# Optimization experiments

Measured on AMD Instinct MI355X. Metric: run time of the kernel, lower is better.

The kernel has to match this reference:

```python
import jax, jax.numpy as jnp
import numpy as np

QN = 127.0  # 2^(8-1)-1, symmetric int8
EPS = 1e-5  # batchnorm eps

def ste_round(v):
    return v + jax.lax.stop_gradient(jnp.round(v) - v)

def quant_act(x):
    # HAWQ-style symmetric per-tensor activation quantization (8-bit)
    s = jnp.maximum(jnp.max(jnp.abs(x)) / QN, 1e-8)
    xq = jnp.clip(ste_round(x / s), -QN - 1.0, QN)
    return xq * s, s

def setup_inputs() -> dict:
    key = jax.random.key(0)
    k1, k2, k3, k4, k5, k6 = jax.random.split(key, 6)
    B, Cin, Cout, H, W = 128, 768, 192, 17, 17
    x = jax.random.normal(k1, (B, Cin, H, W), dtype=jnp.float32)
    conv_w = jax.random.normal(k2, (Cout, Cin, 1, 1), dtype=jnp.float32) * 0.02
    bn_gamma = 1.0 + 0.1 * jax.random.normal(k3, (Cout,), dtype=jnp.float32)
    bn_beta = 0.1 * jax.random.normal(k4, (Cout,), dtype=jnp.float32)
    bn_mean = 0.1 * jax.random.normal(k5, (Cout,), dtype=jnp.float32)
    bn_var = 0.5 + jax.random.uniform(k6, (Cout,), dtype=jnp.float32)
    return {"x": x, "conv_w": conv_w, "bn_gamma": bn_gamma, "bn_beta": bn_beta,
            "bn_mean": bn_mean, "bn_var": bn_var, "cluster": 0}

def reference(x, conv_w, bn_gamma, bn_beta, bn_mean, bn_var, cluster):
    # 1) QuantAct on raw input
    x1, s0 = quant_act(x)
    # 2) QuantAveragePool2d (k=3, s=1, p=1, count_include_pad=True): pool in integer domain
    x_int = ste_round(x1 / s0)
    pooled_sum = jax.lax.reduce_window(x_int, 0.0, jax.lax.add,
                                       (1, 1, 3, 3), (1, 1, 1, 1),
                                       [(0, 0), (0, 0), (1, 1), (1, 1)])
    x2 = (pooled_sum / 9.0) * s0
    # 3) QuantAct after pool
    x3, s1 = quant_act(x2)
    # 4) QuantBnConv2d: fold BN into 1x1 conv, per-channel symmetric weight quant
    std = jnp.sqrt(bn_var + EPS)
    w_fold = conv_w * (bn_gamma / std)[:, None, None, None]          # [O,C,1,1]
    b_fold = bn_beta - bn_gamma * bn_mean / std                      # [O]
    w_sf = jnp.maximum(jnp.max(jnp.abs(w_fold), axis=(1, 2, 3)) / QN, 1e-8)  # [O]
    w_int = jnp.clip(ste_round(w_fold / w_sf[:, None, None, None]), -QN - 1.0, QN)
    xi = x3 / s1                                                     # integer-valued acts
    b_int = ste_round(b_fold / (w_sf * s1))
    out_int = jnp.einsum('bchw,oc->bohw', xi, w_int[:, :, 0, 0]) + b_int[None, :, None, None]
    out = out_int * (w_sf * s1)[None, :, None, None]
    # 5) ReLU + output QuantAct
    out = jax.nn.relu(out)
    outq, s2 = quant_act(out)
    return outq, s2
```

## Files before the change

### kernel.cpp

```cpp
#include <hip/hip_runtime.h>
#include <math.h>

#define B_    128
#define C_    768
#define O_    192
#define HW_   289
#define N_IN  (128*768*289)
#define N_OUT (128*192*289)
#define QN_   127.0f

#define SLAB_E   (32*289)
#define SLAB_SH  9248
#define SLAB_BYT 18496
#define QP_LDS   (32*380)

typedef __attribute__((ext_vector_type(8))) short bf16x8;
typedef __attribute__((ext_vector_type(4))) float f32x4;

#define SWZ(b) ((b) ^ ((((b) >> 6) & 3) << 4))


__global__ void k_absmax_x(const float4* __restrict__ x4, int n4, unsigned* cnt) {
    float m = 0.f;
    const int stride = gridDim.x * blockDim.x;
    int i = blockIdx.x * blockDim.x + threadIdx.x;
    for (; i + stride < n4; i += 2 * stride) {
        float4 v = x4[i];
        float4 w = x4[i + stride];
        m = fmaxf(m, fmaxf(fmaxf(fabsf(v.x), fabsf(v.y)),
                           fmaxf(fabsf(v.z), fabsf(v.w))));
        m = fmaxf(m, fmaxf(fmaxf(fabsf(w.x), fabsf(w.y)),
                           fmaxf(fabsf(w.z), fabsf(w.w))));
    }
    if (i < n4) {
        float4 v = x4[i];
        m = fmaxf(m, fmaxf(fmaxf(fabsf(v.x), fabsf(v.y)),
                           fmaxf(fabsf(v.z), fabsf(v.w))));
    }
#pragma unroll
    for (int off = 32; off; off >>= 1) m = fmaxf(m, __shfl_down(m, off));
    __shared__ float sm[4];
    int lane = threadIdx.x & 63, wv = threadIdx.x >> 6;
    if (lane == 0) sm[wv] = m;
    __syncthreads();
    if (threadIdx.x == 0) {
        float bm = fmaxf(fmaxf(sm[0], sm[1]), fmaxf(sm[2], sm[3]));
        atomicMax(cnt + 0, __float_as_uint(bm));
    }
}

__launch_bounds__(512) __global__
void k_quant_pool(const float* __restrict__ x, short* __restrict__ pooled,
                  unsigned* cnt) {
    __shared__ __align__(16) float fq[QP_LDS + 8];
    __shared__ int smax[8];
    const int tid = threadIdx.x;
    const int kt = blockIdx.x;
    const int b = blockIdx.z;
    const float s0 = fmaxf(__uint_as_float(cnt[0]) / QN_, 1e-8f);

    for (int i = tid; i < QP_LDS + 8; i += 512) fq[i] = 0.f;
    __syncthreads();

    const float4* xg4 = (const float4*)(x + ((size_t)b * 768 + kt * 32) * HW_);
    for (int t = tid; t < SLAB_E / 4; t += 512) {
        float4 v = xg4[t];
        float q0 = rintf(v.x / s0);
        float q1 = rintf(v.y / s0);
        float q2 = rintf(v.z / s0);
        float q3 = rintf(v.w / s0);
        int e = 4 * t;
#pragma unroll
        for (int j = 0; j < 4; ++j) {
            float q = (j == 0) ? q0 : (j == 1) ? q1 : (j == 2) ? q2 : q3;
            int ej = e + j;
            int p = (ej * 29027) >> 23;
            int i2 = ej - p * 289;
            int r = (i2 * 3856) >> 16;
            int c = i2 - r * 17;
            fq[p * 380 + (r + 1) * 20 + (c + 1)] = q;
        }
    }
    __syncthreads();

    short* slab = pooled + (size_t)(b * 24 + kt) * SLAB_SH;
    int tmax = 0;
    for (int task = tid; task < 2720; task += 512) {
        int p = task & 31;
        int rt = task >> 5;
        int r = (rt * 3277) >> 14;
        int t5 = rt - r * 5;
        int c0 = t5 * 4;
        const float* base = fq + p * 380 + r * 20 + c0;
        float4 a0 = *(const float4*)(base);
        float4 a1 = *(const float4*)(base + 4);
        float4 b0 = *(const float4*)(base + 20);
        float4 b1 = *(const float4*)(base + 24);
        float4 d0 = *(const float4*)(base + 40);
        float4 d1 = *(const float4*)(base + 44);
        float s0c = a0.x + b0.x + d0.x;
        float s1c = a0.y + b0.y + d0.y;
        float s2c = a0.z + b0.z + d0.z;
        float s3c = a0.w + b0.w + d0.w;
        float s4c = a1.x + b1.x + d1.x;
        float s5c = a1.y + b1.y + d1.y;
        int o0 = (int)(s0c + s1c + s2c);
        int o1 = (int)(s1c + s2c + s3c);
        int o2 = (int)(s2c + s3c + s4c);
        int o3 = (int)(s3c + s4c + s5c);
        int i0 = r * 17 + c0;
        slab[(i0 + 0) * 32 + p] = (short)o0;
        int a = o0 < 0 ? -o0 : o0; tmax = a > tmax ? a : tmax;
        if (c0 + 1 < 17) {
            slab[(i0 + 1) * 32 + p] = (short)o1;
            a = o1 < 0 ? -o1 : o1; tmax = a > tmax ? a : tmax;
            slab[(i0 + 2) * 32 + p] = (short)o2;
            a = o2 < 0 ? -o2 : o2; tmax = a > tmax ? a : tmax;
            slab[(i0 + 3) * 32 + p] = (short)o3;
            a = o3 < 0 ? -o3 : o3; tmax = a > tmax ? a : tmax;
        }
    }

#pragma unroll
    for (int off = 32; off; off >>= 1) {
        int o = __shfl_down(tmax, off);
        tmax = o > tmax ? o : tmax;
    }
    if ((tid & 63) == 0) smax[tid >> 6] = tmax;
    __syncthreads();
    if (tid == 0) {
        int bm = smax[0];
#pragma unroll
        for (int i = 1; i < 8; ++i) bm = smax[i] > bm ? smax[i] : bm;
        atomicMax((int*)(cnt + 1), bm);
    }
}

__global__ void k_weights(const float* __restrict__ conv_w,
                          const float* __restrict__ g,
                          const float* __restrict__ beta,
                          const float* __restrict__ mu,
                          const float* __restrict__ var,
                          const unsigned* __restrict__ cnt,
                          unsigned short* __restrict__ w_q,
                          float* __restrict__ b_int, float* __restrict__ scale_o,
                          unsigned short* __restrict__ lut) {
    if (blockIdx.x == O_) {
        const float s0 = fmaxf(__uint_as_float(cnt[0]) / QN_, 1e-8f);
        const float maxx2 = ((float)((const int*)cnt)[1] / 9.0f) * s0;
        const float s1 = fmaxf(maxx2 / QN_, 1e-8f);
        for (int i = threadIdx.x; i < 2305; i += 256) {
            float p = (float)(i - 1152);
            float t = (p / 9.0f) * s0;
            float v = rintf(t / s1);
            v = fminf(fmaxf(v, -128.f), 127.f);
            lut[i] = (unsigned short)(__float_as_uint(v) >> 16);
        }
        return;
    }
    const int o = blockIdx.x;
    const float stdv = sqrtf(var[o] + 1e-5f);
    const float r = g[o] / stdv;
    const float* wo = conv_w + o * C_;
    float m = 0.f;
    for (int c = threadIdx.x; c < C_; c += 256) m = fmaxf(m, fabsf(wo[c] * r));
#pragma unroll
    for (int off = 32; off; off >>= 1) m = fmaxf(m, __shfl_down(m, off));
    __shared__ float sm[4];
    __shared__ float swsf;
    int lane = threadIdx.x & 63, wv = threadIdx.x >> 6;
    if (lane == 0) sm[wv] = m;
    __syncthreads();
    if (threadIdx.x == 0) {
        float bm = fmaxf(fmaxf(sm[0], sm[1]), fmaxf(sm[2], sm[3]));
        swsf = fmaxf(bm / QN_, 1e-8f);
    }
    __syncthreads();
    const float wsf = swsf;
    for (int c = threadIdx.x; c < C_; c += 256) {
        float wi = rintf(wo[c] * r / wsf);
        wi = fminf(fmaxf(wi, -128.f), 127.f);
        w_q[(c >> 5) * 6144 + o * 32 + (c & 31)] =
            (unsigned short)(__float_as_uint(wi) >> 16);
    }
    if (threadIdx.x == 0) {
        float s0 = fmaxf(__uint_as_float(cnt[0]) / QN_, 1e-8f);
        float maxx2 = ((float)((const int*)cnt)[1] / 9.0f) * s0;
        float s1 = fmaxf(maxx2 / QN_, 1e-8f);
        float bf = beta[o] - g[o] * mu[o] / stdv;
        b_int[o] = rintf(bf / (wsf * s1));
        scale_o[o] = wsf * s1;
    }
}

__global__ void k_xi(uint4* __restrict__ data,
                     const unsigned short* __restrict__ lut_g) {
    __shared__ unsigned short s_lut[2305];
    for (int i = threadIdx.x; i < 2305; i += 256) s_lut[i] = lut_g[i];
    __syncthreads();
    const int n4 = N_IN / 8;
    for (int i = blockIdx.x * blockDim.x + threadIdx.x; i < n4;
         i += gridDim.x * blockDim.x) {
        uint4 v = data[i];
        uint4 o;
        o.x = (unsigned)s_lut[1152 + (short)(v.x)] |
              ((unsigned)s_lut[1152 + (short)(v.x >> 16)] << 16);
        o.y = (unsigned)s_lut[1152 + (short)(v.y)] |
              ((unsigned)s_lut[1152 + (short)(v.y >> 16)] << 16);
        o.z = (unsigned)s_lut[1152 + (short)(v.z)] |
              ((unsigned)s_lut[1152 + (short)(v.z >> 16)] << 16);
        o.w = (unsigned)s_lut[1152 + (short)(v.w)] |
              ((unsigned)s_lut[1152 + (short)(v.w >> 16)] << 16);
        data[i] = o;
    }
}

__launch_bounds__(256) __global__
void k_gemm(const unsigned short* __restrict__ xi,
            const unsigned short* __restrict__ w_q,
            const float* __restrict__ b_int, const float* __restrict__ scale_o,
            unsigned* cnt, float* __restrict__ out) {
    __shared__ char sW[2][12288];
    __shared__ char sX[2][5120];
    __shared__ float red[4];
    const int tid = threadIdx.x;
    const int b = blockIdx.z;
    const int hw0 = blockIdx.x * 80;
    const int L = tid & 63;
    const int wv = tid >> 6;
    const int wo = wv * 48;
    const char* xi_b = (const char*)xi;

    const int dA = wv * 1024 + L * 16;
    const int rowA = min(hw0 + (dA >> 6), HW_ - 1);
    const int offA = rowA * 64 + ((dA & 63) ^ (((dA >> 6) & 3) << 4));
    const int dB = 4096 + L * 16;
    const int rowB = min(hw0 + (dB >> 6), HW_ - 1);
    const int offB = rowB * 64 + ((dB & 63) ^ (((dB >> 6) & 3) << 4));

    auto stageW = [&](int kt, int buf) {
#pragma unroll
        for (int j = 0; j < 3; ++j) {
            int ldsoff = (wv * 3 + j) * 1024;
            const char* src = (const char*)w_q + kt * 12288 + SWZ(ldsoff + L * 16);
            __builtin_amdgcn_global_load_lds(
                (const __attribute__((address_space(1))) unsigned int*)src,
                (__attribute__((address_space(3))) unsigned int*)(&sW[buf][0] + ldsoff),
                16, 0, 0);
        }
    };
    auto stageX = [&](int kt, int buf) {
        size_t slab = (size_t)(b * 24 + kt) * SLAB_BYT;
        __builtin_amdgcn_global_load_lds(
            (const __attribute__((address_space(1))) unsigned int*)(xi_b + slab + offA),
            (__attribute__((address_space(3))) unsigned int*)(&sX[buf][0] + wv * 1024),
            16, 0, 0);
        if (wv == 0) {
            __builtin_amdgcn_global_load_lds(
                (const __attribute__((address_space(1))) unsigned int*)(xi_b + slab + offB),
                (__attribute__((address_space(3))) unsigned int*)(&sX[buf][0] + 4096),
                16, 0, 0);
        }
    };

    f32x4 acc[3][5] = {};

    stageW(0, 0);
    stageX(0, 0);
    __syncthreads();

    for (int kt = 0; kt < 24; ++kt) {
        const int cur = kt & 1, nxt = cur ^ 1;
        if (kt < 23) {
            stageW(kt + 1, nxt);
            stageX(kt + 1, nxt);
        }
        bf16x8 af[3], bfr[5];
#pragma unroll
        for (int m = 0; m < 3; ++m)
            af[m] = *(const bf16x8*)(&sW[cur][0] +
                SWZ((wo + m * 16 + (L & 15)) * 64 + (L >> 4) * 16));
#pragma unroll
        for (int n = 0; n < 5; ++n)
            bfr[n] = *(const bf16x8*)(&sX[cur][0] +
                SWZ((n * 16 + (L & 15)) * 64 + (L >> 4) * 16));
#pragma unroll
        for (int m = 0; m < 3; ++m)
#pragma unroll
            for (int n = 0; n < 5; ++n)
                acc[m][n] = __builtin_amdgcn_mfma_f32_16x16x32_bf16(
                    af[m], bfr[n], acc[m][n], 0, 0, 0);
        __syncthreads();
    }

    float lmax = 0.f;
#pragma unroll
    for (int m = 0; m < 3; ++m) {
        int ob = wo + m * 16 + (L >> 4) * 4;
        float bi0 = b_int[ob + 0], bi1 = b_int[ob + 1];
        float bi2 = b_int[ob + 2], bi3 = b_int[ob + 3];
        float sc0 = scale_o[ob + 0], sc1 = scale_o[ob + 1];
        float sc2 = scale_o[ob + 2], sc3 = scale_o[ob + 3];
#pragma unroll
        for (int n = 0; n < 5; ++n) {
            int hw = hw0 + n * 16 + (L & 15);
            if (hw < HW_) {
                size_t base = ((size_t)b * O_ + ob) * HW_ + hw;
                float v0 = fmaxf((acc[m][n][0] + bi0) * sc0, 0.f);
                float v1 = fmaxf((acc[m][n][1] + bi1) * sc1, 0.f);
                float v2 = fmaxf((acc[m][n][2] + bi2) * sc2, 0.f);
                float v3 = fmaxf((acc[m][n][3] + bi3) * sc3, 0.f);
                out[base + 0 * HW_] = v0;
                out[base + 1 * HW_] = v1;
                out[base + 2 * HW_] = v2;
                out[base + 3 * HW_] = v3;
                lmax = fmaxf(fmaxf(fmaxf(v0, v1), fmaxf(v2, v3)), lmax);
            }
        }
    }
#pragma unroll
    for (int off = 32; off; off >>= 1) lmax = fmaxf(lmax, __shfl_down(lmax, off));
    if (L == 0) red[wv] = lmax;
    __syncthreads();
    if (tid == 0) {
        float bm = fmaxf(fmaxf(red[0], red[1]), fmaxf(red[2], red[3]));
        atomicMax(cnt + 2, __float_as_uint(bm));
    }
}

__global__ void k_quant_out(float* __restrict__ out, const unsigned* __restrict__ cnt) {
    const float s2 = fmaxf(__uint_as_float(cnt[2]) / QN_, 1e-8f);
    float4* o4 = (float4*)out;
    const int n4 = N_OUT / 4;
    for (int i = blockIdx.x * blockDim.x + threadIdx.x; i < n4;
         i += gridDim.x * blockDim.x) {
        float4 v = o4[i];
        v.x = fminf(fmaxf(rintf(v.x / s2), -128.f), 127.f) * s2;
        v.y = fminf(fmaxf(rintf(v.y / s2), -128.f), 127.f) * s2;
        v.z = fminf(fmaxf(rintf(v.z / s2), -128.f), 127.f) * s2;
        v.w = fminf(fmaxf(rintf(v.w / s2), -128.f), 127.f) * s2;
        o4[i] = v;
    }
    if (blockIdx.x == 0 && threadIdx.x == 0) out[N_OUT] = s2;
}

extern "C" void kernel_launch(void* const* d_in, const int* in_sizes, int n_in,
                              void* d_out, int out_size, void* d_ws, size_t ws_size,
                              hipStream_t stream) {
    const float* x      = (const float*)d_in[0];
    const float* conv_w = (const float*)d_in[1];
    const float* g      = (const float*)d_in[2];
    const float* beta   = (const float*)d_in[3];
    const float* mu     = (const float*)d_in[4];
    const float* var    = (const float*)d_in[5];
    float* out = (float*)d_out;

    char* wsb = (char*)d_ws;
    unsigned* cnt          = (unsigned*)wsb;
    float* b_int           = (float*)(wsb + 1024);
    float* scale_o         = (float*)(wsb + 2048);
    unsigned short* lut    = (unsigned short*)(wsb + 3072);
    unsigned short* w_q    = (unsigned short*)(wsb + 8192);
    short* pooled          = (short*)(wsb + (1u << 20));

    hipMemsetAsync(cnt, 0, 16, stream);
    k_absmax_x<<<2048, 256, 0, stream>>>((const float4*)x, N_IN / 4, cnt);
    dim3 qgrid(24, 1, B_);
    k_quant_pool<<<qgrid, 512, 0, stream>>>(x, pooled, cnt);
    k_weights<<<O_ + 1, 256, 0, stream>>>(conv_w, g, beta, mu, var, cnt, w_q,
                                          b_int, scale_o, lut);
    k_xi<<<2048, 256, 0, stream>>>((uint4*)pooled, lut);
    dim3 ggrid(4, 1, B_);
    k_gemm<<<ggrid, 256, 0, stream>>>((const unsigned short*)pooled, w_q, b_int,
                                      scale_o, cnt, out);
    k_quant_out<<<2048, 256, 0, stream>>>(out, cnt);
}
```

Measured before the change: 152.8 us.

## Fuse LUT requantization of pooled activations into GEMM X-tile staging

Removes the standalone k_xi pass that rewrote the pooled int16 buffer into bf16 integer activations through a lookup table. The GEMM now loads raw pooled values into registers, maps them through an LDS copy of the LUT, and writes the swizzled bf16 tile into shared memory after the MFMA block, keeping the double buffering. This avoids a full read-modify-write of the roughly 57 MB activation buffer and one kernel launch. In exchange, X staging moves from async global-to-LDS loads to register loads plus LDS gathers, which adds latency and VALU/LDS work inside the GEMM loop.

```diff
diff --git a/kernel.cpp b/kernel.cpp
--- a/kernel.cpp
+++ b/kernel.cpp
@@ -193,35 +193,15 @@
     }
 }
 
-__global__ void k_xi(uint4* __restrict__ data,
-                     const unsigned short* __restrict__ lut_g) {
-    __shared__ unsigned short s_lut[2305];
-    for (int i = threadIdx.x; i < 2305; i += 256) s_lut[i] = lut_g[i];
-    __syncthreads();
-    const int n4 = N_IN / 8;
-    for (int i = blockIdx.x * blockDim.x + threadIdx.x; i < n4;
-         i += gridDim.x * blockDim.x) {
-        uint4 v = data[i];
-        uint4 o;
-        o.x = (unsigned)s_lut[1152 + (short)(v.x)] |
-              ((unsigned)s_lut[1152 + (short)(v.x >> 16)] << 16);
-        o.y = (unsigned)s_lut[1152 + (short)(v.y)] |
-              ((unsigned)s_lut[1152 + (short)(v.y >> 16)] << 16);
-        o.z = (unsigned)s_lut[1152 + (short)(v.z)] |
-              ((unsigned)s_lut[1152 + (short)(v.z >> 16)] << 16);
-        o.w = (unsigned)s_lut[1152 + (short)(v.w)] |
-              ((unsigned)s_lut[1152 + (short)(v.w >> 16)] << 16);
-        data[i] = o;
-    }
-}
-
 __launch_bounds__(256) __global__
-void k_gemm(const unsigned short* __restrict__ xi,
+void k_gemm(const short* __restrict__ pooled,
             const unsigned short* __restrict__ w_q,
+            const unsigned short* __restrict__ lut_g,
             const float* __restrict__ b_int, const float* __restrict__ scale_o,
             unsigned* cnt, float* __restrict__ out) {
     __shared__ char sW[2][12288];
     __shared__ char sX[2][5120];
+    __shared__ unsigned short s_lut[2305];
     __shared__ float red[4];
     const int tid = threadIdx.x;
     const int b = blockIdx.z;
@@ -229,14 +209,16 @@
     const int L = tid & 63;
     const int wv = tid >> 6;
     const int wo = wv * 48;
-    const char* xi_b = (const char*)xi;
-
-    const int dA = wv * 1024 + L * 16;
-    const int rowA = min(hw0 + (dA >> 6), HW_ - 1);
-    const int offA = rowA * 64 + ((dA & 63) ^ (((dA >> 6) & 3) << 4));
-    const int dB = 4096 + L * 16;
-    const int rowB = min(hw0 + (dB >> 6), HW_ - 1);
-    const int offB = rowB * 64 + ((dB & 63) ^ (((dB >> 6) & 3) << 4));
+    const char* pooled_b = (const char*)pooled;
+
+    for (int i = tid; i < 2305; i += 256) s_lut[i] = lut_g[i];
+
+    const int hwr0 = tid >> 2, cg0 = tid & 3;
+    const int hwr1 = 64 + (tid >> 2), cg1 = tid & 3;
+    const bool act1 = tid < 64;
+    const int hwg0 = hw0 + hwr0, hwg1 = hw0 + hwr1;
+
+    uint4 xr0, xr1;
 
     auto stageW = [&](int kt, int buf) {
 #pragma unroll
@@ -249,31 +231,53 @@
                 16, 0, 0);
         }
     };
-    auto stageX = [&](int kt, int buf) {
+    auto loadX = [&](int kt) {
+        uint4 z; z.x = z.y = z.z = z.w = 0u;
         size_t slab = (size_t)(b * 24 + kt) * SLAB_BYT;
-        __builtin_amdgcn_global_load_lds(
-            (const __attribute__((address_space(1))) unsigned int*)(xi_b + slab + offA),
-            (__attribute__((address_space(3))) unsigned int*)(&sX[buf][0] + wv * 1024),
-            16, 0, 0);
-        if (wv == 0) {
-            __builtin_amdgcn_global_load_lds(
-                (const __attribute__((address_space(1))) unsigned int*)(xi_b + slab + offB),
-                (__attribute__((address_space(3))) unsigned int*)(&sX[buf][0] + 4096),
-                16, 0, 0);
-        }
+        xr0 = (hwg0 < HW_)
+            ? *(const uint4*)(pooled_b + slab + hwg0 * 64 + cg0 * 16) : z;
+        if (act1)
+            xr1 = (hwg1 < HW_)
+                ? *(const uint4*)(pooled_b + slab + hwg1 * 64 + cg1 * 16) : z;
     };
+    auto writeX = [&](int buf) {
+        uint4 q;
+        q.x = (unsigned)s_lut[1152 + (short)(xr0.x)] |
+              ((unsigned)s_lut[1152 + (short)(xr0.x >> 16)] << 16);
+        q.y = (unsigned)s_lut[1152 + (short)(xr0.y)] |
+              ((unsigned)s_lut[1152 + (short)(xr0.y >> 16)] << 16);
+        q.z = (unsigned)s_lut[1152 + (short)(xr0.z)] |
+              ((unsigned)s_lut[1152 + (short)(xr0.z >> 16)] << 16);
+        q.w = (unsigned)s_lut[1152 + (short)(xr0.w)] |
+              ((unsigned)s_lut[1152 + (short)(xr0.w >> 16)] << 16);
+        *(uint4*)(&sX[buf][0] + SWZ(hwr0 * 64 + cg0 * 16)) = q;
+        if (act1) {
+            uint4 p2;
+            p2.x = (unsigned)s_lut[1152 + (short)(xr1.x)] |
+                   ((unsigned)s_lut[1152 + (short)(xr1.x >> 16)] << 16);
+            p2.y = (unsigned)s_lut[1152 + (short)(xr1.y)] |
+                   ((unsigned)s_lut[1152 + (short)(xr1.y >> 16)] << 16);
+            p2.z = (unsigned)s_lut[1152 + (short)(xr1.z)] |
+                   ((unsigned)s_lut[1152 + (short)(xr1.z >> 16)] << 16);
+            p2.w = (unsigned)s_lut[1152 + (short)(xr1.w)] |
+                   ((unsigned)s_lut[1152 + (short)(xr1.w >> 16)] << 16);
+            *(uint4*)(&sX[buf][0] + SWZ(hwr1 * 64 + cg1 * 16)) = p2;
+        }
+    };
 
     f32x4 acc[3][5] = {};
 
     stageW(0, 0);
-    stageX(0, 0);
+    loadX(0);
+    __syncthreads();
+    writeX(0);
     __syncthreads();
 
     for (int kt = 0; kt < 24; ++kt) {
         const int cur = kt & 1, nxt = cur ^ 1;
         if (kt < 23) {
             stageW(kt + 1, nxt);
-            stageX(kt + 1, nxt);
+            loadX(kt + 1);
         }
         bf16x8 af[3], bfr[5];
 #pragma unroll
@@ -290,6 +294,7 @@
             for (int n = 0; n < 5; ++n)
                 acc[m][n] = __builtin_amdgcn_mfma_f32_16x16x32_bf16(
                     af[m], bfr[n], acc[m][n], 0, 0, 0);
+        if (kt < 23) writeX(nxt);
         __syncthreads();
     }
 
@@ -369,9 +374,7 @@
     k_quant_pool<<<qgrid, 512, 0, stream>>>(x, pooled, cnt);
     k_weights<<<O_ + 1, 256, 0, stream>>>(conv_w, g, beta, mu, var, cnt, w_q,
                                           b_int, scale_o, lut);
-    k_xi<<<2048, 256, 0, stream>>>((uint4*)pooled, lut);
     dim3 ggrid(4, 1, B_);
-    k_gemm<<<ggrid, 256, 0, stream>>>((const unsigned short*)pooled, w_q, b_int,
-                                      scale_o, cnt, out);
+    k_gemm<<<ggrid, 256, 0, stream>>>(pooled, w_q, lut, b_int, scale_o, cnt, out);
     k_quant_out<<<2048, 256, 0, stream>>>(out, cnt);
 }
```

Result: faster. 143.6 us (-6.1%).
